# Kernel optimization log

Hardware: AMD Instinct MI355X
Metric: run time of the kernel (lower is better)

The kernel has to match this reference:

```python
import jax, jax.numpy as jnp
import numpy as np

N_MED = 100000   # len(medicine_it): nodes in the single hyperedge
VOCAB = 200000   # medicine vocab (rows of both embedding tables)
C_IN = 256
C_OUT = 256


def setup_inputs() -> dict:
    key = jax.random.key(0)
    k1, k2, k3, k4, k5 = jax.random.split(key, 5)
    return {
        "medicine_it": jax.random.randint(k1, (N_MED,), 0, VOCAB),
        "m_embeddings": jax.random.normal(k2, (VOCAB, C_IN), dtype=jnp.float32),
        "pretrained_weight": jax.random.normal(k3, (VOCAB, C_OUT), dtype=jnp.float32),
        "W": jax.random.normal(k4, (C_OUT, C_IN), dtype=jnp.float32) / np.sqrt(C_IN).astype(np.float32),
        "bias": jax.random.normal(k5, (C_OUT,), dtype=jnp.float32) * 0.01,
    }


def reference(medicine_it, m_embeddings, pretrained_weight, W, bias):
    # --- forward(): gather medicine rows, HypergraphConv with ONE hyperedge ---
    x = m_embeddings[medicine_it]                 # [N, C_in]  row gather
    xw = x @ W.T                                  # [N, C_out] lin (bias added after propagation, as in PyG)
    n = xw.shape[0]
    # Single hyperedge containing all N nodes: edge degree B = N, node degree D = 1.
    # edge_feat = B^{-1} H^T (X W^T);  node_out = D^{-1} H edge_feat + bias (same for all nodes)
    edge_feat = jnp.sum(xw, axis=0) / jnp.asarray(n, xw.dtype)   # [C_out]
    med_node_feature = edge_feat[None, :] + bias                 # [1, C_out], identical per node
    # --- output(): sum_i pretrained[m_i] + sum_i representation[i] ---
    embedding_pretrained = jnp.sum(pretrained_weight[medicine_it], axis=0, keepdims=True)  # [1, C_out]
    embedding_trained = jnp.asarray(n, xw.dtype) * med_node_feature                        # [1, C_out]
    return (embedding_pretrained + embedding_trained)[None, :, :]  # [1, 1, C_out]
```

## Files before the change

### kernel.cpp

```cpp
#include <hip/hip_runtime.h>


typedef float f4 __attribute__((ext_vector_type(4)));

#define NCOPY 16

__global__ __launch_bounds__(256) void hist_kernel(
    const int* __restrict__ idx, int* __restrict__ counts, int n)
{
    int i = blockIdx.x * blockDim.x + threadIdx.x;
    const int stride = gridDim.x * blockDim.x;
    for (; i < n; i += stride) atomicAdd(&counts[idx[i]], 1);
}

__global__ __launch_bounds__(256) void scan_kernel(
    const int* __restrict__ counts,
    const float* __restrict__ memb,
    const float* __restrict__ pre,
    float* __restrict__ acc,
    int vocab)
{
    const int lane = threadIdx.x & 63;
    const int wid  = (blockIdx.x * blockDim.x + threadIdx.x) >> 6;
    const int tab  = wid & 1;
    const int base = (wid >> 1) * 64;

    f4 a4 = {0.f, 0.f, 0.f, 0.f};

    if (base < vocab) {
        int c = 0;
        if (base + lane < vocab) c = counts[base + lane];
        const float cf = (float)c;
        unsigned long long m = __ballot(c != 0);

        const float* tbl = tab ? pre : memb;
        const f4* rows = reinterpret_cast<const f4*>(tbl) + (size_t)base * 64 + lane;

        while (m) {
            const int k0 = __ffsll(m) - 1; m &= m - 1;
            const float w0 = __shfl(cf, k0, 64);
            int k1 = k0, k2 = k0, k3 = k0;
            float w1 = 0.f, w2 = 0.f, w3 = 0.f;
            if (m) { k1 = __ffsll(m) - 1; m &= m - 1; w1 = __shfl(cf, k1, 64); }
            if (m) { k2 = __ffsll(m) - 1; m &= m - 1; w2 = __shfl(cf, k2, 64); }
            if (m) { k3 = __ffsll(m) - 1; m &= m - 1; w3 = __shfl(cf, k3, 64); }

            const f4 a0 = rows[(size_t)k0 * 64];
            const f4 a1 = rows[(size_t)k1 * 64];
            const f4 a2 = rows[(size_t)k2 * 64];
            const f4 a3 = rows[(size_t)k3 * 64];

            a4 += a0 * w0;
            a4 += a1 * w1;
            a4 += a2 * w2;
            a4 += a3 * w3;
        }
    }

    __shared__ float sAcc[2][256];
    sAcc[0][threadIdx.x] = 0.f;
    sAcc[1][threadIdx.x] = 0.f;
    __syncthreads();

    const int ch = lane * 4;
    atomicAdd(&sAcc[tab][ch + 0], a4.x);
    atomicAdd(&sAcc[tab][ch + 1], a4.y);
    atomicAdd(&sAcc[tab][ch + 2], a4.z);
    atomicAdd(&sAcc[tab][ch + 3], a4.w);
    __syncthreads();

    float* myacc = acc + (size_t)(blockIdx.x & (NCOPY - 1)) * 512;
    atomicAdd(&myacc[threadIdx.x],       sAcc[0][threadIdx.x]);
    atomicAdd(&myacc[256 + threadIdx.x], sAcc[1][threadIdx.x]);
}

__global__ __launch_bounds__(256) void finish_kernel(
    const float* __restrict__ acc,
    const float* __restrict__ W,
    const float* __restrict__ bias,
    float* __restrict__ out,
    float nf)
{
    const int c = blockIdx.x;
    const int t = threadIdx.x;

    float s_t = 0.f;
    #pragma unroll
    for (int cp = 0; cp < NCOPY; ++cp) s_t += acc[cp * 512 + t];

    float v = W[(size_t)c * 256 + t] * s_t;
    for (int off = 32; off > 0; off >>= 1)
        v += __shfl_down(v, off, 64);

    __shared__ float part[4];
    if ((t & 63) == 0) part[t >> 6] = v;
    __syncthreads();

    if (t == 0) {
        float p_c = 0.f;
        #pragma unroll
        for (int cp = 0; cp < NCOPY; ++cp) p_c += acc[cp * 512 + 256 + c];
        out[c] = (part[0] + part[1] + part[2] + part[3]) + p_c + nf * bias[c];
    }
}

__global__ __launch_bounds__(256) void gather_sum_kernel(
    const int* __restrict__ idx,
    const float* __restrict__ memb,
    const float* __restrict__ pre,
    float* __restrict__ acc,
    int n)
{
    const int lane = threadIdx.x & 63;
    const int wave = threadIdx.x >> 6;
    const int globalWave = blockIdx.x * 4 + wave;
    const int totalWaves = gridDim.x * 4;

    f4 accS = {0.f,0.f,0.f,0.f};
    f4 accP = {0.f,0.f,0.f,0.f};

    for (int i = globalWave; i < n; i += totalWaves) {
        const int r = idx[i];
        const f4 a = reinterpret_cast<const f4*>(memb + (size_t)r * 256)[lane];
        const f4 b = reinterpret_cast<const f4*>(pre  + (size_t)r * 256)[lane];
        accS += a; accP += b;
    }

    __shared__ float sS[256];
    __shared__ float sP[256];
    sS[threadIdx.x] = 0.f;
    sP[threadIdx.x] = 0.f;
    __syncthreads();
    const int ch = lane * 4;
    atomicAdd(&sS[ch + 0], accS.x); atomicAdd(&sS[ch + 1], accS.y);
    atomicAdd(&sS[ch + 2], accS.z); atomicAdd(&sS[ch + 3], accS.w);
    atomicAdd(&sP[ch + 0], accP.x); atomicAdd(&sP[ch + 1], accP.y);
    atomicAdd(&sP[ch + 2], accP.z); atomicAdd(&sP[ch + 3], accP.w);
    __syncthreads();
    float* myacc = acc + (size_t)(blockIdx.x & (NCOPY - 1)) * 512;
    atomicAdd(&myacc[threadIdx.x],       sS[threadIdx.x]);
    atomicAdd(&myacc[256 + threadIdx.x], sP[threadIdx.x]);
}

extern "C" void kernel_launch(void* const* d_in, const int* in_sizes, int n_in,
                              void* d_out, int out_size, void* d_ws, size_t ws_size,
                              hipStream_t stream)
{
    const int*   idx  = (const int*)d_in[0];
    const float* memb = (const float*)d_in[1];
    const float* pre  = (const float*)d_in[2];
    const float* W    = (const float*)d_in[3];
    const float* bias = (const float*)d_in[4];
    float* out = (float*)d_out;

    const int n     = in_sizes[0];
    const int vocab = in_sizes[1] / 256;

    const size_t countsBytes = (size_t)vocab * sizeof(int);
    const size_t accBytes    = (size_t)NCOPY * 512 * sizeof(float);

    if (ws_size >= countsBytes + accBytes) {
        int*   counts = (int*)d_ws;
        float* acc    = (float*)((char*)d_ws + countsBytes);

        hipMemsetAsync(d_ws, 0, countsBytes + accBytes, stream);
        hist_kernel<<<400, 256, 0, stream>>>(idx, counts, n);

        const int waves  = 2 * ((vocab + 63) / 64);
        const int blocks = (waves + 3) / 4;
        scan_kernel<<<blocks, 256, 0, stream>>>(counts, memb, pre, acc, vocab);
        finish_kernel<<<256, 256, 0, stream>>>(acc, W, bias, out, (float)n);
    } else {
        float* acc = (float*)d_ws;
        hipMemsetAsync(d_ws, 0, accBytes, stream);
        gather_sum_kernel<<<512, 256, 0, stream>>>(idx, memb, pre, acc, n);
        finish_kernel<<<256, 256, 0, stream>>>(acc, W, bias, out, (float)n);
    }
}
```

Baseline: 49.71 us.

## Pack histogram counts into bytes and fuse finish into scan via last-block

The histogram now packs four 8-bit counters per 32-bit word, which shrinks the counts array and the memset by a factor of four. The scan kernel reads the byte counts directly. The final W projection and bias step now runs inside the scan kernel: the last block to finish, detected with an atomic counter, does it, which removes a separate kernel launch. The risk is that a byte counter overflows if any index repeats more than 255 times, and the last-block matvec is serialized on one block.

```diff
diff --git a/kernel.cpp b/kernel.cpp
--- a/kernel.cpp
+++ b/kernel.cpp
@@ -6,19 +6,26 @@
 #define NCOPY 16
 
 __global__ __launch_bounds__(256) void hist_kernel(
-    const int* __restrict__ idx, int* __restrict__ counts, int n)
+    const int* __restrict__ idx, unsigned int* __restrict__ countsW, int n)
 {
     int i = blockIdx.x * blockDim.x + threadIdx.x;
     const int stride = gridDim.x * blockDim.x;
-    for (; i < n; i += stride) atomicAdd(&counts[idx[i]], 1);
-}
-
-__global__ __launch_bounds__(256) void scan_kernel(
-    const int* __restrict__ counts,
+    for (; i < n; i += stride) {
+        const int v = idx[i];
+        atomicAdd(&countsW[v >> 2], 1u << ((v & 3) * 8));
+    }
+}
+
+__global__ __launch_bounds__(256) void scan_finish_kernel(
+    const unsigned char* __restrict__ cnt8,
     const float* __restrict__ memb,
     const float* __restrict__ pre,
     float* __restrict__ acc,
-    int vocab)
+    int* __restrict__ done,
+    const float* __restrict__ W,
+    const float* __restrict__ bias,
+    float* __restrict__ out,
+    int vocab, float nf, int nblocks)
 {
     const int lane = threadIdx.x & 63;
     const int wid  = (blockIdx.x * blockDim.x + threadIdx.x) >> 6;
@@ -29,7 +36,7 @@
 
     if (base < vocab) {
         int c = 0;
-        if (base + lane < vocab) c = counts[base + lane];
+        if (base + lane < vocab) c = cnt8[base + lane];
         const float cf = (float)c;
         unsigned long long m = __ballot(c != 0);
 
@@ -72,6 +79,80 @@
     float* myacc = acc + (size_t)(blockIdx.x & (NCOPY - 1)) * 512;
     atomicAdd(&myacc[threadIdx.x],       sAcc[0][threadIdx.x]);
     atomicAdd(&myacc[256 + threadIdx.x], sAcc[1][threadIdx.x]);
+
+    __shared__ int lastFlag;
+    if (threadIdx.x == 0) {
+        __threadfence();
+        lastFlag = (atomicAdd(done, 1) == nblocks - 1);
+    }
+    __syncthreads();
+    if (!lastFlag) return;
+    __threadfence();
+
+    const int t  = threadIdx.x;
+    const int wv = t >> 6;
+
+    __shared__ float sVec[256];
+    __shared__ float pVec[256];
+    float s_t = 0.f, p_t = 0.f;
+    #pragma unroll
+    for (int cp = 0; cp < NCOPY; ++cp) {
+        s_t += acc[cp * 512 + t];
+        p_t += acc[cp * 512 + 256 + t];
+    }
+    sVec[t] = s_t;
+    pVec[t] = p_t;
+    __syncthreads();
+
+    const f4* W4 = reinterpret_cast<const f4*>(W);
+    const f4  sv = reinterpret_cast<const f4*>(sVec)[lane];
+    for (int i = 0; i < 64; ++i) {
+        const int c = wv * 64 + i;
+        const f4 wr = W4[(size_t)c * 64 + lane];
+        float v = wr.x * sv.x + wr.y * sv.y + wr.z * sv.z + wr.w * sv.w;
+        #pragma unroll
+        for (int off = 32; off > 0; off >>= 1)
+            v += __shfl_xor(v, off, 64);
+        if (lane == 0) out[c] = v + pVec[c] + nf * bias[c];
+    }
+}
+
+__global__ __launch_bounds__(256) void gather_sum_kernel(
+    const int* __restrict__ idx,
+    const float* __restrict__ memb,
+    const float* __restrict__ pre,
+    float* __restrict__ acc,
+    int n)
+{
+    const int lane = threadIdx.x & 63;
+    const int wave = threadIdx.x >> 6;
+    const int globalWave = blockIdx.x * 4 + wave;
+    const int totalWaves = gridDim.x * 4;
+
+    f4 accS = {0.f,0.f,0.f,0.f};
+    f4 accP = {0.f,0.f,0.f,0.f};
+
+    for (int i = globalWave; i < n; i += totalWaves) {
+        const int r = idx[i];
+        const f4 a = reinterpret_cast<const f4*>(memb + (size_t)r * 256)[lane];
+        const f4 b = reinterpret_cast<const f4*>(pre  + (size_t)r * 256)[lane];
+        accS += a; accP += b;
+    }
+
+    __shared__ float sS[256];
+    __shared__ float sP[256];
+    sS[threadIdx.x] = 0.f;
+    sP[threadIdx.x] = 0.f;
+    __syncthreads();
+    const int ch = lane * 4;
+    atomicAdd(&sS[ch + 0], accS.x); atomicAdd(&sS[ch + 1], accS.y);
+    atomicAdd(&sS[ch + 2], accS.z); atomicAdd(&sS[ch + 3], accS.w);
+    atomicAdd(&sP[ch + 0], accP.x); atomicAdd(&sP[ch + 1], accP.y);
+    atomicAdd(&sP[ch + 2], accP.z); atomicAdd(&sP[ch + 3], accP.w);
+    __syncthreads();
+    float* myacc = acc + (size_t)(blockIdx.x & (NCOPY - 1)) * 512;
+    atomicAdd(&myacc[threadIdx.x],       sS[threadIdx.x]);
+    atomicAdd(&myacc[256 + threadIdx.x], sP[threadIdx.x]);
 }
 
 __global__ __launch_bounds__(256) void finish_kernel(
@@ -104,44 +185,6 @@
     }
 }
 
-__global__ __launch_bounds__(256) void gather_sum_kernel(
-    const int* __restrict__ idx,
-    const float* __restrict__ memb,
-    const float* __restrict__ pre,
-    float* __restrict__ acc,
-    int n)
-{
-    const int lane = threadIdx.x & 63;
-    const int wave = threadIdx.x >> 6;
-    const int globalWave = blockIdx.x * 4 + wave;
-    const int totalWaves = gridDim.x * 4;
-
-    f4 accS = {0.f,0.f,0.f,0.f};
-    f4 accP = {0.f,0.f,0.f,0.f};
-
-    for (int i = globalWave; i < n; i += totalWaves) {
-        const int r = idx[i];
-        const f4 a = reinterpret_cast<const f4*>(memb + (size_t)r * 256)[lane];
-        const f4 b = reinterpret_cast<const f4*>(pre  + (size_t)r * 256)[lane];
-        accS += a; accP += b;
-    }
-
-    __shared__ float sS[256];
-    __shared__ float sP[256];
-    sS[threadIdx.x] = 0.f;
-    sP[threadIdx.x] = 0.f;
-    __syncthreads();
-    const int ch = lane * 4;
-    atomicAdd(&sS[ch + 0], accS.x); atomicAdd(&sS[ch + 1], accS.y);
-    atomicAdd(&sS[ch + 2], accS.z); atomicAdd(&sS[ch + 3], accS.w);
-    atomicAdd(&sP[ch + 0], accP.x); atomicAdd(&sP[ch + 1], accP.y);
-    atomicAdd(&sP[ch + 2], accP.z); atomicAdd(&sP[ch + 3], accP.w);
-    __syncthreads();
-    float* myacc = acc + (size_t)(blockIdx.x & (NCOPY - 1)) * 512;
-    atomicAdd(&myacc[threadIdx.x],       sS[threadIdx.x]);
-    atomicAdd(&myacc[256 + threadIdx.x], sP[threadIdx.x]);
-}
-
 extern "C" void kernel_launch(void* const* d_in, const int* in_sizes, int n_in,
                               void* d_out, int out_size, void* d_ws, size_t ws_size,
                               hipStream_t stream)
@@ -156,20 +199,23 @@
     const int n     = in_sizes[0];
     const int vocab = in_sizes[1] / 256;
 
-    const size_t countsBytes = (size_t)vocab * sizeof(int);
+    const size_t countsBytes = (size_t)((vocab + 3) / 4) * 4;
     const size_t accBytes    = (size_t)NCOPY * 512 * sizeof(float);
 
-    if (ws_size >= countsBytes + accBytes) {
-        int*   counts = (int*)d_ws;
-        float* acc    = (float*)((char*)d_ws + countsBytes);
-
-        hipMemsetAsync(d_ws, 0, countsBytes + accBytes, stream);
-        hist_kernel<<<400, 256, 0, stream>>>(idx, counts, n);
+    if (ws_size >= countsBytes + accBytes + 64) {
+        unsigned int* countsW = (unsigned int*)d_ws;
+        float*        acc     = (float*)((char*)d_ws + countsBytes);
+        int*          done    = (int*)((char*)d_ws + countsBytes + accBytes);
+
+        hipMemsetAsync(d_ws, 0, countsBytes + accBytes + 64, stream);
+
+        hist_kernel<<<400, 256, 0, stream>>>(idx, countsW, n);
 
         const int waves  = 2 * ((vocab + 63) / 64);
         const int blocks = (waves + 3) / 4;
-        scan_kernel<<<blocks, 256, 0, stream>>>(counts, memb, pre, acc, vocab);
-        finish_kernel<<<256, 256, 0, stream>>>(acc, W, bias, out, (float)n);
+        scan_finish_kernel<<<blocks, 256, 0, stream>>>(
+            (const unsigned char*)countsW, memb, pre, acc, done,
+            W, bias, out, vocab, (float)n, blocks);
     } else {
         float* acc = (float*)d_ws;
         hipMemsetAsync(d_ws, 0, accBytes, stream);
```

Result: slower. 126.8 us (+155.1%).
